# Performance work log

Measured on AMD Instinct MI355X. Metric: run time of the kernel, lower is better.

## Reference

```python
import jax, jax.numpy as jnp
import numpy as np

H = 128   # hidden_size
B = 8
TQ = 512  # num queries
TK = 512  # num keys


def setup_inputs() -> dict:
    key = jax.random.key(0)
    ks = jax.random.split(key, 8)
    s = 1.0 / np.sqrt(H)  # torch Linear default init bound
    return {
        "queries": jax.random.normal(ks[0], (B, TQ, H), dtype=jnp.float32),
        "keys": jax.random.normal(ks[1], (B, TK, H), dtype=jnp.float32),
        "Wa_w": jax.random.uniform(ks[2], (H, H), jnp.float32, -s, s),
        "Wa_b": jax.random.uniform(ks[3], (H,), jnp.float32, -s, s),
        "Ua_w": jax.random.uniform(ks[4], (H, H), jnp.float32, -s, s),
        "Ua_b": jax.random.uniform(ks[5], (H,), jnp.float32, -s, s),
        "Va_w": jax.random.uniform(ks[6], (H,), jnp.float32, -s, s),
        "Va_b": jax.random.uniform(ks[7], (), jnp.float32, -s, s),
    }


def reference(queries, keys, Wa_w, Wa_b, Ua_w, Ua_b, Va_w, Va_b):
    # Linear projections (torch Linear: y = x @ W.T + b)
    q = queries @ Wa_w.T + Wa_b                  # (B, Tq, H)
    k = keys @ Ua_w.T + Ua_b                     # (B, Tk, H)
    # Additive (Bahdanau) scores with broadcast intermediate (B, Tq, Tk, H)
    e = jnp.tanh(q[:, :, None, :] + k[:, None, :, :])
    scores = jnp.einsum('bqkh,h->bqk', e, Va_w) + Va_b  # (B, Tq, Tk)
    weights = jax.nn.softmax(scores, axis=-1)            # softmax over keys
    contexts = jnp.einsum('bqk,bkh->bqh', weights, keys) # (B, Tq, H)
    return contexts, weights
```

## Files before the change

kernel.cpp:

```cpp
#include <hip/hip_runtime.h>
#include <hip/hip_bf16.h>
#include <stdint.h>

#define HD 128
#define NB 8
#define TQN 512
#define TKN 512
#define QT 8
#define KTILE 64
#define KSTR 132
#define QSTR 132
#define KBSTR 136

typedef __attribute__((ext_vector_type(8))) short short8;
typedef __attribute__((ext_vector_type(4))) float f32x4;
typedef __attribute__((ext_vector_type(2))) float f32x2;

#if __has_builtin(__builtin_elementwise_fma)
#define FMA2(a,b,c) __builtin_elementwise_fma((a),(b),(c))
#else
#define FMA2(a,b,c) ((a)*(b)+(c))
#endif

static __device__ __forceinline__ float lo16(uint32_t w){
  union { uint32_t i; float f; } v; v.i = w << 16; return v.f;
}
static __device__ __forceinline__ float hi16(uint32_t w){
  union { uint32_t i; float f; } v; v.i = w & 0xffff0000u; return v.f;
}
static __device__ __forceinline__ float bf2f(unsigned short u){
  union { uint32_t i; float f; } v; v.i = ((uint32_t)u) << 16; return v.f;
}
static __device__ __forceinline__ uint32_t f2bf(float f){
  union { float f; uint32_t i; } v; v.f = f;
  uint32_t u = v.i;
  u += 0x7fffu + ((u >> 16) & 1u);
  return u >> 16;
}
static __device__ __forceinline__ float tanh_acc(float x){
  float e = __builtin_amdgcn_exp2f(x * 2.8853900817779268f);
  return fmaf(-2.0f, __builtin_amdgcn_rcpf(e + 1.0f), 1.0f);
}
template<int CTRL>
static __device__ __forceinline__ float dpp_add(float x){
  union { float f; int i; } u; u.f = x;
  int y = __builtin_amdgcn_update_dpp(0, u.i, CTRL, 0xf, 0xf, true);
  union { int i; float f; } w; w.i = y;
  return x + w.f;
}
static __device__ __forceinline__ float ld1(const void* p, size_t idx, bool f32){
  return f32 ? ((const float*)p)[idx] : bf2f(((const unsigned short*)p)[idx]);
}
static __device__ __forceinline__ short8 ld8bf(const void* p, size_t idx, bool f32){
  short8 r;
  if (f32){
    const float* s = (const float*)p + idx;
    #pragma unroll
    for (int i = 0; i < 8; i++) r[i] = (short)f2bf(s[i]);
  } else {
    r = *(const short8*)((const unsigned short*)p + idx);
  }
  return r;
}

__global__ __launch_bounds__(256) void proj_kernel(
    const void* __restrict__ queries, const void* __restrict__ keys,
    const void* __restrict__ Wa_w,   const void* __restrict__ Wa_b,
    const void* __restrict__ Ua_w,   const void* __restrict__ Ua_b,
    float* __restrict__ tq_g, float* __restrict__ tk_g)
{
  __shared__ unsigned int flg_s[8];
  const int tid = threadIdx.x;
  if (tid < 8) flg_s[tid] = 0;
  __syncthreads();
  {
    const void* ptrs[6] = {queries, keys, Wa_w, Wa_b, Ua_w, Ua_b};
    const int grp = tid >> 5;
    const int l   = tid & 31;
    if (grp < 6){
      const unsigned short* p = (const unsigned short*)ptrs[grp];
      unsigned short a = p[2*l], c = p[64 + 2*l];
      if (((a >> 7) & 0xFF) > 0x90 || ((c >> 7) & 0xFF) > 0x90)
        atomicOr(&flg_s[grp], 1u);
    }
  }
  __syncthreads();
  const int lane = tid & 63, wv = tid >> 6, ln = lane & 15, quad = lane >> 4;
  const int b7  = blockIdx.x & 7;
  const int idx = blockIdx.x >> 3;
  const int row0 = (idx < 32) ? (b7*TQN + idx*16)
                              : (NB*TQN + b7*TKN + (idx-32)*16);

  const void* x; const void* W; const void* bias; float* dst; int r;
  bool fx, fw, fb;
  if (row0 < NB*TQN){
    x = queries; W = Wa_w; bias = Wa_b; dst = tq_g; r = row0;
    fx = flg_s[0] != 0; fw = flg_s[2] != 0; fb = flg_s[3] != 0;
  } else {
    x = keys; W = Ua_w; bias = Ua_b; dst = tk_g; r = row0 - NB*TQN;
    fx = flg_s[1] != 0; fw = flg_s[4] != 0; fb = flg_s[5] != 0;
  }

  short8 a[4];
  #pragma unroll
  for (int ks = 0; ks < 4; ks++)
    a[ks] = ld8bf(x, (size_t)(r + ln)*HD + ks*32 + quad*8, fx);

  #pragma unroll
  for (int nt = 0; nt < 2; nt++){
    const int h0 = (2*wv + nt)*16;
    f32x4 c = {0.f,0.f,0.f,0.f};
    #pragma unroll
    for (int ks = 0; ks < 4; ks++)
      c = __builtin_amdgcn_mfma_f32_16x16x32_bf16(
            a[ks], ld8bf(W, (size_t)(h0 + ln)*HD + ks*32 + quad*8, fw), c, 0,0,0);
    const float wb = ld1(bias, h0 + ln, fb);
    #pragma unroll
    for (int r4 = 0; r4 < 4; r4++){
      const float e = __builtin_amdgcn_exp2f((c[r4] + wb) * 2.8853900817779268f);
      dst[(size_t)(r + quad*4 + r4)*HD + h0 + ln] =
          fminf(fmaxf(e, 0x1p-13f), 0x1p13f);
    }
  }
}

__global__ __launch_bounds__(512, 4) void attn_kernel(
    const void* __restrict__ queries, const void* __restrict__ keys,
    const void* __restrict__ Va_w,
    const float* __restrict__ tq_g, const float* __restrict__ tk_g,
    void* __restrict__ out)
{
  __shared__ __align__(16) float tk_s[KTILE*KSTR];
  __shared__ float sc_s[QT*TKN];
  __shared__ unsigned int flg_s[4];

  const int tid = threadIdx.x;
  const int b     = blockIdx.x & 7;
  const int qbase = (blockIdx.x >> 3) * QT;

  float4 st[4];
  {
    const float4* src = (const float4*)(tk_g + (size_t)(b*TKN)*HD);
    #pragma unroll
    for (int j = 0; j < 4; j++) st[j] = src[tid + 512*j];
  }

  if (tid < 4) flg_s[tid] = 0;
  __syncthreads();
  {
    const void* ptrs[3] = {queries, keys, Va_w};
    const int grp = tid >> 5;
    const int l   = tid & 31;
    if (grp < 3){
      const unsigned short* p = (const unsigned short*)ptrs[grp];
      unsigned short a = p[2*l], c = p[64 + 2*l];
      if (((a >> 7) & 0xFF) > 0x90 || ((c >> 7) & 0xFF) > 0x90)
        atomicOr(&flg_s[grp], 1u);
    }
  }
  __syncthreads();
  const bool fQ  = flg_s[0] != 0;
  const bool fK  = flg_s[1] != 0;
  const bool fVw = flg_s[2] != 0;

  const int lane = tid & 63;
  const int wv   = tid >> 6;
  const int ln   = lane & 15;
  const int quad = lane >> 4;
  const int s8   = lane >> 3;
  const int o8   = lane & 7;

  f32x2 eq2[8], a2[8];
  {
    const float* qsrc = tq_g + (size_t)(b*TQN + qbase + wv)*HD + o8*16;
    #pragma unroll
    for (int c = 0; c < 4; c++){
      const float4 t = *(const float4*)(qsrc + c*4);
      eq2[2*c].x = t.x; eq2[2*c].y = t.y;
      eq2[2*c+1].x = t.z; eq2[2*c+1].y = t.w;
      a2[2*c].x   = -2.0f * ld1(Va_w, o8*16 + c*4 + 0, fVw);
      a2[2*c].y   = -2.0f * ld1(Va_w, o8*16 + c*4 + 1, fVw);
      a2[2*c+1].x = -2.0f * ld1(Va_w, o8*16 + c*4 + 2, fVw);
      a2[2*c+1].y = -2.0f * ld1(Va_w, o8*16 + c*4 + 3, fVw);
    }
  }
  f32x2 one2; one2.x = 1.f; one2.y = 1.f;

  float sc8[8];
  for (int kt = 0; kt < 8; kt++){
    #pragma unroll
    for (int j = 0; j < 4; j++){
      const int f = tid + 512*j;
      *(float4*)(tk_s + (f >> 5)*KSTR + (f & 31)*4) = st[j];
    }
    __syncthreads();
    if (kt < 7){
      const float4* src = (const float4*)(tk_g + (size_t)(b*TKN + (kt+1)*KTILE)*HD);
      #pragma unroll
      for (int j = 0; j < 4; j++) st[j] = src[tid + 512*j];
    }

    float acc[8];
    #pragma unroll
    for (int i = 0; i < 8; i++){
      const float* tk = tk_s + (i*8 + s8)*KSTR + o8*16;
      float acci = 0.f;
      #pragma unroll
      for (int c = 0; c < 4; c++){
        const float4 kv = *(const float4*)(tk + c*4);
        f32x2 kv0; kv0.x = kv.x; kv0.y = kv.y;
        f32x2 kv1; kv1.x = kv.z; kv1.y = kv.w;
        f32x2 x01 = FMA2(eq2[2*c],   kv0, one2);
        f32x2 x23 = FMA2(eq2[2*c+1], kv1, one2);
        f32x2 xs01; xs01.x = x01.y; xs01.y = x01.x;
        f32x2 xs23; xs23.x = x23.y; xs23.y = x23.x;
        f32x2 s01 = a2[2*c]   * xs01;
        f32x2 s23 = a2[2*c+1] * xs23;
        const float p01 = x01.x * x01.y;
        const float p23 = x23.x * x23.y;
        const float n01 = s01.x + s01.y;
        const float n23 = s23.x + s23.y;
        const float P   = p01 * p23;
        const float N   = fmaf(n01, p23, n23 * p01);
        acci = fmaf(N, __builtin_amdgcn_rcpf(P), acci);
      }
      acc[i] = acci;
    }
    #pragma unroll
    for (int i = 0; i < 8; i++){
      float a = acc[i];
      a = dpp_add<0xB1>(a);
      a = dpp_add<0x4E>(a);
      a = dpp_add<0x141>(a);
      acc[i] = a;
    }
    float sc = acc[0];
    #pragma unroll
    for (int i = 1; i < 8; i++) sc = (o8 == i) ? acc[i] : sc;
    sc8[kt] = sc;
    __syncthreads();
  }

  {
    float m = sc8[0];
    #pragma unroll
    for (int j = 1; j < 8; j++) m = fmaxf(m, sc8[j]);
    #pragma unroll
    for (int o = 32; o > 0; o >>= 1) m = fmaxf(m, __shfl_xor(m, o));
    float sum = 0.f;
    #pragma unroll
    for (int j = 0; j < 8; j++){
      sc8[j] = __builtin_amdgcn_exp2f((sc8[j]-m)*1.4426950408889634f);
      sum += sc8[j];
    }
    #pragma unroll
    for (int o = 32; o > 0; o >>= 1) sum += __shfl_xor(sum, o);
    const float inv = __builtin_amdgcn_rcpf(sum);
    const int psrc = ((((lane & 7) << 3) | (lane >> 3)) << 2);
    const size_t wbase = (size_t)NB*TQN*HD + (size_t)(b*TQN + qbase + wv)*TKN;
    #pragma unroll
    for (int j = 0; j < 8; j++){
      union { float f; int i; } u; u.f = sc8[j]*inv;
      union { int i; float f; } t; t.i = __builtin_amdgcn_ds_bpermute(psrc, u.i);
      sc_s[wv*TKN + j*64 + lane] = t.f;
      if (fQ) ((float*)out)[wbase + j*64 + lane] = t.f;
      else    ((unsigned short*)out)[wbase + j*64 + lane] = (unsigned short)f2bf(t.f);
    }
  }
  __syncthreads();

  {
    const int p2 = wv & 3;
    const int g2 = wv >> 2;
    const int h0 = ln * 8;
    f32x2 a0v[4], a1v[4];
    #pragma unroll
    for (int t = 0; t < 4; t++){
      a0v[t].x = 0.f; a0v[t].y = 0.f;
      a1v[t].x = 0.f; a1v[t].y = 0.f;
    }
    const float* w0rb = sc_s + (2*p2)*TKN + g2*32;
    if (!fK){
      const unsigned short* kb = (const unsigned short*)keys
          + (size_t)(b*TKN + g2*32)*HD + h0;
      for (int kt = 0; kt < 8; kt++){
        const float* w0r = w0rb + kt*KTILE;
        const float* w1r = w0r + TKN;
        #pragma unroll
        for (int i = 0; i < 8; i++){
          const int k = i*4 + quad;
          const uint4 v = *(const uint4*)(kb + (size_t)(kt*KTILE + k)*HD);
          const float w0 = w0r[k];
          const float w1 = w1r[k];
          f32x2 c0; c0.x = lo16(v.x); c0.y = hi16(v.x);
          f32x2 c1; c1.x = lo16(v.y); c1.y = hi16(v.y);
          f32x2 c2; c2.x = lo16(v.z); c2.y = hi16(v.z);
          f32x2 c3; c3.x = lo16(v.w); c3.y = hi16(v.w);
          f32x2 w0v; w0v.x = w0; w0v.y = w0;
          f32x2 w1v; w1v.x = w1; w1v.y = w1;
          a0v[0] = FMA2(w0v, c0, a0v[0]); a0v[1] = FMA2(w0v, c1, a0v[1]);
          a0v[2] = FMA2(w0v, c2, a0v[2]); a0v[3] = FMA2(w0v, c3, a0v[3]);
          a1v[0] = FMA2(w1v, c0, a1v[0]); a1v[1] = FMA2(w1v, c1, a1v[1]);
          a1v[2] = FMA2(w1v, c2, a1v[2]); a1v[3] = FMA2(w1v, c3, a1v[3]);
        }
      }
    } else {
      const float* kb = (const float*)keys + (size_t)(b*TKN + g2*32)*HD + h0;
      for (int kt = 0; kt < 8; kt++){
        const float* w0r = w0rb + kt*KTILE;
        const float* w1r = w0r + TKN;
        #pragma unroll
        for (int i = 0; i < 8; i++){
          const int k = i*4 + quad;
          const float* kr = kb + (size_t)(kt*KTILE + k)*HD;
          const float4 k0 = *(const float4*)(kr);
          const float4 k1 = *(const float4*)(kr + 4);
          const float w0 = w0r[k];
          const float w1 = w1r[k];
          f32x2 c0; c0.x = k0.x; c0.y = k0.y;
          f32x2 c1; c1.x = k0.z; c1.y = k0.w;
          f32x2 c2; c2.x = k1.x; c2.y = k1.y;
          f32x2 c3; c3.x = k1.z; c3.y = k1.w;
          f32x2 w0v; w0v.x = w0; w0v.y = w0;
          f32x2 w1v; w1v.x = w1; w1v.y = w1;
          a0v[0] = FMA2(w0v, c0, a0v[0]); a0v[1] = FMA2(w0v, c1, a0v[1]);
          a0v[2] = FMA2(w0v, c2, a0v[2]); a0v[3] = FMA2(w0v, c3, a0v[3]);
          a1v[0] = FMA2(w1v, c0, a1v[0]); a1v[1] = FMA2(w1v, c1, a1v[1]);
          a1v[2] = FMA2(w1v, c2, a1v[2]); a1v[3] = FMA2(w1v, c3, a1v[3]);
        }
      }
    }
    float a0[8], a1[8];
    #pragma unroll
    for (int t = 0; t < 4; t++){
      a0[2*t] = a0v[t].x; a0[2*t+1] = a0v[t].y;
      a1[2*t] = a1v[t].x; a1[2*t+1] = a1v[t].y;
    }
    #pragma unroll
    for (int t = 0; t < 8; t++){
      a0[t] += __shfl_xor(a0[t], 16); a0[t] += __shfl_xor(a0[t], 32);
      a1[t] += __shfl_xor(a1[t], 16); a1[t] += __shfl_xor(a1[t], 32);
    }
    __syncthreads();
    float* part = sc_s;
    if (g2 == 1 && quad == 0){
      *(float4*)(part + (2*p2  )*HD + h0    ) = (float4){a0[0],a0[1],a0[2],a0[3]};
      *(float4*)(part + (2*p2  )*HD + h0 + 4) = (float4){a0[4],a0[5],a0[6],a0[7]};
      *(float4*)(part + (2*p2+1)*HD + h0    ) = (float4){a1[0],a1[1],a1[2],a1[3]};
      *(float4*)(part + (2*p2+1)*HD + h0 + 4) = (float4){a1[4],a1[5],a1[6],a1[7]};
    }
    __syncthreads();
    if (g2 == 0 && quad == 0){
      const float4 p00 = *(const float4*)(part + (2*p2  )*HD + h0    );
      const float4 p01 = *(const float4*)(part + (2*p2  )*HD + h0 + 4);
      const float4 p10 = *(const float4*)(part + (2*p2+1)*HD + h0    );
      const float4 p11 = *(const float4*)(part + (2*p2+1)*HD + h0 + 4);
      const size_t crow0 = (size_t)(b*TQN + qbase + 2*p2    )*HD + h0;
      const size_t crow1 = (size_t)(b*TQN + qbase + 2*p2 + 1)*HD + h0;
      if (fQ){
        float* oc = (float*)out;
        *(float4*)(oc + crow0)     = (float4){a0[0]+p00.x, a0[1]+p00.y, a0[2]+p00.z, a0[3]+p00.w};
        *(float4*)(oc + crow0 + 4) = (float4){a0[4]+p01.x, a0[5]+p01.y, a0[6]+p01.z, a0[7]+p01.w};
        *(float4*)(oc + crow1)     = (float4){a1[0]+p10.x, a1[1]+p10.y, a1[2]+p10.z, a1[3]+p10.w};
        *(float4*)(oc + crow1 + 4) = (float4){a1[4]+p11.x, a1[5]+p11.y, a1[6]+p11.z, a1[7]+p11.w};
      } else {
        uint4 o0, o1;
        o0.x = f2bf(a0[0]+p00.x) | (f2bf(a0[1]+p00.y) << 16);
        o0.y = f2bf(a0[2]+p00.z) | (f2bf(a0[3]+p00.w) << 16);
        o0.z = f2bf(a0[4]+p01.x) | (f2bf(a0[5]+p01.y) << 16);
        o0.w = f2bf(a0[6]+p01.z) | (f2bf(a0[7]+p01.w) << 16);
        o1.x = f2bf(a1[0]+p10.x) | (f2bf(a1[1]+p10.y) << 16);
        o1.y = f2bf(a1[2]+p10.z) | (f2bf(a1[3]+p10.w) << 16);
        o1.z = f2bf(a1[4]+p11.x) | (f2bf(a1[5]+p11.y) << 16);
        o1.w = f2bf(a1[6]+p11.z) | (f2bf(a1[7]+p11.w) << 16);
        *(uint4*)((unsigned short*)out + crow0) = o0;
        *(uint4*)((unsigned short*)out + crow1) = o1;
      }
    }
  }
}

__global__ __launch_bounds__(512, 4) void fused_kernel(
    const void* __restrict__ queries, const void* __restrict__ keys,
    const void* __restrict__ Wa_w,   const void* __restrict__ Wa_b,
    const void* __restrict__ Ua_w,   const void* __restrict__ Ua_b,
    const void* __restrict__ Va_w,
    void* __restrict__ out)
{
  __shared__ float qp_s[QT*QSTR];
  __shared__ float va_s[HD];
  __shared__ __align__(16) unsigned short keys_s[KTILE*KBSTR];
  __shared__ __align__(16) float kp_s[KTILE*KSTR];
  __shared__ float sc_s[QT*TKN];
  __shared__ unsigned int flg_s[8];

  const int tid = threadIdx.x;
  if (tid < 8) flg_s[tid] = 0;
  __syncthreads();
  {
    const void* ptrs[7] = {queries, keys, Wa_w, Wa_b, Ua_w, Ua_b, Va_w};
    const int grp = tid >> 5;
    const int l   = tid & 31;
    if (grp < 7){
      const unsigned short* p = (const unsigned short*)ptrs[grp];
      unsigned short a = p[2*l], c = p[64 + 2*l];
      if (((a >> 7) & 0xFF) > 0x90 || ((c >> 7) & 0xFF) > 0x90)
        atomicOr(&flg_s[grp], 1u);
    }
  }
  __syncthreads();
  const bool fQ  = flg_s[0] != 0;
  const bool fK  = flg_s[1] != 0;
  const bool fWw = flg_s[2] != 0;
  const bool fWb = flg_s[3] != 0;
  const bool fUw = flg_s[4] != 0;
  const bool fUb = flg_s[5] != 0;
  const bool fVw = flg_s[6] != 0;

  const int lane = tid & 63;
  const int wv   = tid >> 6;
  const int ln   = lane & 15;
  const int quad = lane >> 4;
  const int b     = blockIdx.x >> 6;
  const int qbase = (blockIdx.x & 63) * QT;

  if (tid < HD) va_s[tid] = ld1(Va_w, tid, fVw);
  {
    const int h0 = wv * 16;
    const size_t qrow = (size_t)(b*TQN + qbase + (ln & 7))*HD;
    f32x4 c = {0.f,0.f,0.f,0.f};
    #pragma unroll
    for (int ks = 0; ks < 4; ks++){
      short8 a = ld8bf(queries, qrow + ks*32 + quad*8, fQ);
      short8 w = ld8bf(Wa_w, (size_t)(h0 + ln)*HD + ks*32 + quad*8, fWw);
      c = __builtin_amdgcn_mfma_f32_16x16x32_bf16(a, w, c, 0,0,0);
    }
    const float wb = ld1(Wa_b, h0 + ln, fWb);
    #pragma unroll
    for (int r = 0; r < 4; r++){
      const int row = quad*4 + r;
      if (row < QT) qp_s[row*QSTR + h0 + ln] = tanh_acc(c[r] + wb);
    }
  }
  short8 ub[4];
  float ubias;
  {
    const int h0 = wv * 16;
    #pragma unroll
    for (int ks = 0; ks < 4; ks++)
      ub[ks] = ld8bf(Ua_w, (size_t)(h0 + ln)*HD + ks*32 + quad*8, fUw);
    ubias = ld1(Ua_b, h0 + ln, fUb);
  }
  {
    if (fK){
      const float4* src = (const float4*)((const float*)keys + (size_t)(b*TKN)*HD);
      #pragma unroll
      for (int j = 0; j < 4; j++){
        const int f = tid + 512*j;
        float4 v = src[f];
        const int k = f >> 5, h = (f & 31)*4;
        uint2 p;
        p.x = f2bf(v.x) | (f2bf(v.y) << 16);
        p.y = f2bf(v.z) | (f2bf(v.w) << 16);
        *(uint2*)(keys_s + k*KBSTR + h) = p;
      }
    } else {
      const uint4* src = (const uint4*)((const unsigned short*)keys + (size_t)(b*TKN)*HD);
      #pragma unroll
      for (int j = 0; j < 2; j++){
        const int f = tid + 512*j;
        uint4 v = src[f];
        const int k = f >> 4, h = (f & 15)*8;
        *(uint4*)(keys_s + k*KBSTR + h) = v;
      }
    }
  }
  __syncthreads();

  const int s8 = lane >> 3;
  const int o8 = lane & 7;
  float tqr[16], var[16], vat[16];
  {
    const float* qsrc = qp_s + wv*QSTR + o8*16;
    const float* vsrc = va_s + o8*16;
    #pragma unroll
    for (int c = 0; c < 4; c++){
      float4 t = *(const float4*)(qsrc + c*4);
      float4 v = *(const float4*)(vsrc + c*4);
      tqr[c*4+0]=t.x; tqr[c*4+1]=t.y; tqr[c*4+2]=t.z; tqr[c*4+3]=t.w;
      var[c*4+0]=v.x; var[c*4+1]=v.y; var[c*4+2]=v.z; var[c*4+3]=v.w;
      vat[c*4+0]=v.x*t.x; vat[c*4+1]=v.y*t.y; vat[c*4+2]=v.z*t.z; vat[c*4+3]=v.w*t.w;
    }
  }
  for (int kt = 0; kt < 8; kt++){
    f32x4 kc[4];
    #pragma unroll
    for (int mt = 0; mt < 4; mt++) kc[mt] = (f32x4){0.f,0.f,0.f,0.f};
    #pragma unroll
    for (int ks = 0; ks < 4; ks++){
      short8 af[4];
      #pragma unroll
      for (int mt = 0; mt < 4; mt++)
        af[mt] = *(const short8*)(keys_s + (mt*16 + ln)*KBSTR + ks*32 + quad*8);
      #pragma unroll
      for (int mt = 0; mt < 4; mt++)
        kc[mt] = __builtin_amdgcn_mfma_f32_16x16x32_bf16(af[mt], ub[ks], kc[mt], 0,0,0);
    }
    __syncthreads();
    #pragma unroll
    for (int mt = 0; mt < 4; mt++)
      #pragma unroll
      for (int r = 0; r < 4; r++)
        kp_s[(mt*16 + quad*4 + r)*KSTR + wv*16 + ln] = tanh_acc(kc[mt][r] + ubias);
    if (kt < 7){
      if (fK){
        const float4* src = (const float4*)((const float*)keys + (size_t)(b*TKN + (kt+1)*KTILE)*HD);
        #pragma unroll
        for (int j = 0; j < 4; j++){
          const int f = tid + 512*j;
          float4 v = src[f];
          const int k = f >> 5, h = (f & 31)*4;
          uint2 p;
          p.x = f2bf(v.x) | (f2bf(v.y) << 16);
          p.y = f2bf(v.z) | (f2bf(v.w) << 16);
          *(uint2*)(keys_s + k*KBSTR + h) = p;
        }
      } else {
        const uint4* src = (const uint4*)((const unsigned short*)keys + (size_t)(b*TKN + (kt+1)*KTILE)*HD);
        #pragma unroll
        for (int j = 0; j < 2; j++){
          const int f = tid + 512*j;
          uint4 v = src[f];
          const int k = f >> 4, h = (f & 15)*8;
          *(uint4*)(keys_s + k*KBSTR + h) = v;
        }
      }
    }
    __syncthreads();
    float acc[8];
    #pragma unroll
    for (int i = 0; i < 8; i++) acc[i] = 0.f;
    #pragma unroll
    for (int i = 0; i < 8; i++){
      const float* tk = kp_s + (i*8 + s8)*KSTR + o8*16;
      #pragma unroll
      for (int c = 0; c < 4; c++){
        const float4 kv = *(const float4*)(tk + c*4);
        acc[i] = fmaf(fmaf(var[c*4+0], kv.x, vat[c*4+0]),
                      __builtin_amdgcn_rcpf(fmaf(tqr[c*4+0], kv.x, 1.f)), acc[i]);
        acc[i] = fmaf(fmaf(var[c*4+1], kv.y, vat[c*4+1]),
                      __builtin_amdgcn_rcpf(fmaf(tqr[c*4+1], kv.y, 1.f)), acc[i]);
        acc[i] = fmaf(fmaf(var[c*4+2], kv.z, vat[c*4+2]),
                      __builtin_amdgcn_rcpf(fmaf(tqr[c*4+2], kv.z, 1.f)), acc[i]);
        acc[i] = fmaf(fmaf(var[c*4+3], kv.w, vat[c*4+3]),
                      __builtin_amdgcn_rcpf(fmaf(tqr[c*4+3], kv.w, 1.f)), acc[i]);
      }
    }
    #pragma unroll
    for (int i = 0; i < 8; i++){
      float a = acc[i];
      a = dpp_add<0xB1>(a);
      a = dpp_add<0x4E>(a);
      a = dpp_add<0x141>(a);
      acc[i] = a;
    }
    float sc = acc[0];
    #pragma unroll
    for (int i = 1; i < 8; i++) sc = (o8 == i) ? acc[i] : sc;
    sc_s[wv*TKN + kt*KTILE + o8*8 + s8] = sc;
  }
  __syncthreads();
  {
    float vals[8];
    float m = -1e30f;
    #pragma unroll
    for (int j = 0; j < 8; j++){
      vals[j] = sc_s[wv*TKN + lane + 64*j];
      m = fmaxf(m, vals[j]);
    }
    #pragma unroll
    for (int o = 32; o > 0; o >>= 1) m = fmaxf(m, __shfl_xor(m, o));
    float sum = 0.f;
    #pragma unroll
    for (int j = 0; j < 8; j++){
      vals[j] = __builtin_amdgcn_exp2f((vals[j]-m)*1.4426950408889634f);
      sum += vals[j];
    }
    #pragma unroll
    for (int o = 32; o > 0; o >>= 1) sum += __shfl_xor(sum, o);
    const float inv = __builtin_amdgcn_rcpf(sum);
    const size_t wbase = (size_t)NB*TQN*HD + (size_t)(b*TQN + qbase + wv)*TKN;
    #pragma unroll
    for (int j = 0; j < 8; j++){
      const float w = vals[j]*inv;
      sc_s[wv*TKN + lane + 64*j] = w;
      if (fQ) ((float*)out)[wbase + lane + 64*j] = w;
      else    ((unsigned short*)out)[wbase + lane + 64*j] = (unsigned short)f2bf(w);
    }
  }
  __syncthreads();
  {
    const int p2 = wv & 3;
    const int g2 = wv >> 2;
    const int h0 = ln * 8;
    float a0[8], a1[8];
    #pragma unroll
    for (int t = 0; t < 8; t++){ a0[t] = 0.f; a1[t] = 0.f; }
    for (int kt = 0; kt < 8; kt++){
      if (fK){
        const float4* src = (const float4*)((const float*)keys + (size_t)(b*TKN + kt*KTILE)*HD);
        #pragma unroll
        for (int j = 0; j < 4; j++){
          const int f = tid + 512*j;
          const int k = f >> 5, h = (f & 31)*4;
          *(float4*)(kp_s + k*KSTR + h) = src[f];
        }
      } else {
        const uint4* src = (const uint4*)((const unsigned short*)keys + (size_t)(b*TKN + kt*KTILE)*HD);
        #pragma unroll
        for (int j = 0; j < 2; j++){
          const int f = tid + 512*j;
          const int k = f >> 4, h = (f & 15)*8;
          uint4 v = src[f];
          float4 d0, d1;
          d0.x = lo16(v.x); d0.y = hi16(v.x); d0.z = lo16(v.y); d0.w = hi16(v.y);
          d1.x = lo16(v.z); d1.y = hi16(v.z); d1.z = lo16(v.w); d1.w = hi16(v.w);
          *(float4*)(kp_s + k*KSTR + h)     = d0;
          *(float4*)(kp_s + k*KSTR + h + 4) = d1;
        }
      }
      __syncthreads();
      const float* w0r = sc_s + (2*p2)*TKN + kt*KTILE + g2*32;
      const float* w1r = w0r + TKN;
      #pragma unroll
      for (int i = 0; i < 8; i++){
        const int k = i*4 + quad;
        const float w0 = w0r[k];
        const float w1 = w1r[k];
        const float* kr = kp_s + (g2*32 + k)*KSTR + h0;
        const float4 k0 = *(const float4*)(kr);
        const float4 k1 = *(const float4*)(kr + 4);
        a0[0]=fmaf(w0,k0.x,a0[0]); a0[1]=fmaf(w0,k0.y,a0[1]);
        a0[2]=fmaf(w0,k0.z,a0[2]); a0[3]=fmaf(w0,k0.w,a0[3]);
        a0[4]=fmaf(w0,k1.x,a0[4]); a0[5]=fmaf(w0,k1.y,a0[5]);
        a0[6]=fmaf(w0,k1.z,a0[6]); a0[7]=fmaf(w0,k1.w,a0[7]);
        a1[0]=fmaf(w1,k0.x,a1[0]); a1[1]=fmaf(w1,k0.y,a1[1]);
        a1[2]=fmaf(w1,k0.z,a1[2]); a1[3]=fmaf(w1,k0.w,a1[3]);
        a1[4]=fmaf(w1,k1.x,a1[4]); a1[5]=fmaf(w1,k1.y,a1[5]);
        a1[6]=fmaf(w1,k1.z,a1[6]); a1[7]=fmaf(w1,k1.w,a1[7]);
      }
      __syncthreads();
    }
    #pragma unroll
    for (int t = 0; t < 8; t++){
      a0[t] += __shfl_xor(a0[t], 16); a0[t] += __shfl_xor(a0[t], 32);
      a1[t] += __shfl_xor(a1[t], 16); a1[t] += __shfl_xor(a1[t], 32);
    }
    float* part = qp_s;
    if (g2 == 1 && quad == 0){
      *(float4*)(part + (2*p2  )*HD + h0    ) = (float4){a0[0],a0[1],a0[2],a0[3]};
      *(float4*)(part + (2*p2  )*HD + h0 + 4) = (float4){a0[4],a0[5],a0[6],a0[7]};
      *(float4*)(part + (2*p2+1)*HD + h0    ) = (float4){a1[0],a1[1],a1[2],a1[3]};
      *(float4*)(part + (2*p2+1)*HD + h0 + 4) = (float4){a1[4],a1[5],a1[6],a1[7]};
    }
    __syncthreads();
    if (g2 == 0 && quad == 0){
      const float4 p00 = *(const float4*)(part + (2*p2  )*HD + h0    );
      const float4 p01 = *(const float4*)(part + (2*p2  )*HD + h0 + 4);
      const float4 p10 = *(const float4*)(part + (2*p2+1)*HD + h0    );
      const float4 p11 = *(const float4*)(part + (2*p2+1)*HD + h0 + 4);
      const size_t crow0 = (size_t)(b*TQN + qbase + 2*p2    )*HD + h0;
      const size_t crow1 = (size_t)(b*TQN + qbase + 2*p2 + 1)*HD + h0;
      if (fQ){
        float* oc = (float*)out;
        *(float4*)(oc + crow0)     = (float4){a0[0]+p00.x, a0[1]+p00.y, a0[2]+p00.z, a0[3]+p00.w};
        *(float4*)(oc + crow0 + 4) = (float4){a0[4]+p01.x, a0[5]+p01.y, a0[6]+p01.z, a0[7]+p01.w};
        *(float4*)(oc + crow1)     = (float4){a1[0]+p10.x, a1[1]+p10.y, a1[2]+p10.z, a1[3]+p10.w};
        *(float4*)(oc + crow1 + 4) = (float4){a1[4]+p11.x, a1[5]+p11.y, a1[6]+p11.z, a1[7]+p11.w};
      } else {
        uint4 o0, o1;
        o0.x = f2bf(a0[0]+p00.x) | (f2bf(a0[1]+p00.y) << 16);
        o0.y = f2bf(a0[2]+p00.z) | (f2bf(a0[3]+p00.w) << 16);
        o0.z = f2bf(a0[4]+p01.x) | (f2bf(a0[5]+p01.y) << 16);
        o0.w = f2bf(a0[6]+p01.z) | (f2bf(a0[7]+p01.w) << 16);
        o1.x = f2bf(a1[0]+p10.x) | (f2bf(a1[1]+p10.y) << 16);
        o1.y = f2bf(a1[2]+p10.z) | (f2bf(a1[3]+p10.w) << 16);
        o1.z = f2bf(a1[4]+p11.x) | (f2bf(a1[5]+p11.y) << 16);
        o1.w = f2bf(a1[6]+p11.z) | (f2bf(a1[7]+p11.w) << 16);
        *(uint4*)((unsigned short*)out + crow0) = o0;
        *(uint4*)((unsigned short*)out + crow1) = o1;
      }
    }
  }
}

extern "C" void kernel_launch(void* const* d_in, const int* in_sizes, int n_in,
                              void* d_out, int out_size, void* d_ws, size_t ws_size,
                              hipStream_t stream) {
  (void)in_sizes; (void)n_in; (void)out_size;
  const size_t need = (size_t)2 * NB * TQN * HD * sizeof(float);
  if (ws_size >= need){
    float* tq_g = (float*)d_ws;
    float* tk_g = tq_g + (size_t)NB*TQN*HD;
    proj_kernel<<<512, 256, 0, stream>>>(d_in[0], d_in[1], d_in[2], d_in[3],
                                         d_in[4], d_in[5], tq_g, tk_g);
    attn_kernel<<<512, 512, 0, stream>>>(d_in[0], d_in[1], d_in[6],
                                         tq_g, tk_g, d_out);
  } else {
    fused_kernel<<<512, 512, 0, stream>>>(d_in[0], d_in[1], d_in[2], d_in[3],
                                          d_in[4], d_in[5], d_in[6], d_out);
  }
}
```

Baseline: 151.2 us.

## Halve queries per block, split hidden dim across waves, drop score LDS buffer

```diff
diff --git a/kernel.cpp b/kernel.cpp
--- a/kernel.cpp
+++ b/kernel.cpp
@@ -6,11 +6,13 @@
 #define NB 8
 #define TQN 512
 #define TKN 512
-#define QT 8
+#define QT 4
 #define KTILE 64
 #define KSTR 132
 #define QSTR 132
 #define KBSTR 136
+#define FQT 8
+#define WGT_OFF 2048
 
 typedef __attribute__((ext_vector_type(8))) short short8;
 typedef __attribute__((ext_vector_type(4))) float f32x4;
@@ -124,14 +126,13 @@
   }
 }
 
-__global__ __launch_bounds__(512, 4) void attn_kernel(
+__global__ __launch_bounds__(512, 8) void attn_kernel(
     const void* __restrict__ queries, const void* __restrict__ keys,
     const void* __restrict__ Va_w,
     const float* __restrict__ tq_g, const float* __restrict__ tk_g,
     void* __restrict__ out)
 {
   __shared__ __align__(16) float tk_s[KTILE*KSTR];
-  __shared__ float sc_s[QT*TKN];
   __shared__ unsigned int flg_s[4];
 
   const int tid = threadIdx.x;
@@ -165,23 +166,25 @@
 
   const int lane = tid & 63;
   const int wv   = tid >> 6;
+  const int qr   = wv & 3;
+  const int hh   = wv >> 2;
   const int ln   = lane & 15;
   const int quad = lane >> 4;
   const int s8   = lane >> 3;
   const int o8   = lane & 7;
 
-  f32x2 eq2[8], a2[8];
-  {
-    const float* qsrc = tq_g + (size_t)(b*TQN + qbase + wv)*HD + o8*16;
-    #pragma unroll
-    for (int c = 0; c < 4; c++){
+  f32x2 eq2[4], a2[4];
+  {
+    const float* qsrc = tq_g + (size_t)(b*TQN + qbase + qr)*HD + o8*16 + hh*8;
+    #pragma unroll
+    for (int c = 0; c < 2; c++){
       const float4 t = *(const float4*)(qsrc + c*4);
       eq2[2*c].x = t.x; eq2[2*c].y = t.y;
       eq2[2*c+1].x = t.z; eq2[2*c+1].y = t.w;
-      a2[2*c].x   = -2.0f * ld1(Va_w, o8*16 + c*4 + 0, fVw);
-      a2[2*c].y   = -2.0f * ld1(Va_w, o8*16 + c*4 + 1, fVw);
-      a2[2*c+1].x = -2.0f * ld1(Va_w, o8*16 + c*4 + 2, fVw);
-      a2[2*c+1].y = -2.0f * ld1(Va_w, o8*16 + c*4 + 3, fVw);
+      a2[2*c].x   = -2.0f * ld1(Va_w, o8*16 + hh*8 + c*4 + 0, fVw);
+      a2[2*c].y   = -2.0f * ld1(Va_w, o8*16 + hh*8 + c*4 + 1, fVw);
+      a2[2*c+1].x = -2.0f * ld1(Va_w, o8*16 + hh*8 + c*4 + 2, fVw);
+      a2[2*c+1].y = -2.0f * ld1(Va_w, o8*16 + hh*8 + c*4 + 3, fVw);
     }
   }
   f32x2 one2; one2.x = 1.f; one2.y = 1.f;
@@ -203,10 +206,10 @@
     float acc[8];
     #pragma unroll
     for (int i = 0; i < 8; i++){
-      const float* tk = tk_s + (i*8 + s8)*KSTR + o8*16;
+      const float* tk = tk_s + (i*8 + s8)*KSTR + o8*16 + hh*8;
       float acci = 0.f;
       #pragma unroll
-      for (int c = 0; c < 4; c++){
+      for (int c = 0; c < 2; c++){
         const float4 kv = *(const float4*)(tk + c*4);
         f32x2 kv0; kv0.x = kv.x; kv0.y = kv.y;
         f32x2 kv1; kv1.x = kv.z; kv1.y = kv.w;
@@ -241,28 +244,39 @@
     __syncthreads();
   }
 
-  {
-    float m = sc8[0];
-    #pragma unroll
-    for (int j = 1; j < 8; j++) m = fmaxf(m, sc8[j]);
+  if (hh == 1){
+    #pragma unroll
+    for (int kt = 0; kt < 8; kt++)
+      tk_s[qr*TKN + kt*64 + o8*8 + s8] = sc8[kt];
+  }
+  __syncthreads();
+  if (hh == 0){
+    float vals[8];
+    float m = -1e30f;
+    #pragma unroll
+    for (int j = 0; j < 8; j++){
+      vals[j] = sc8[j] + tk_s[qr*TKN + j*64 + o8*8 + s8];
+      m = fmaxf(m, vals[j]);
+    }
     #pragma unroll
     for (int o = 32; o > 0; o >>= 1) m = fmaxf(m, __shfl_xor(m, o));
     float sum = 0.f;
     #pragma unroll
     for (int j = 0; j < 8; j++){
-      sc8[j] = __builtin_amdgcn_exp2f((sc8[j]-m)*1.4426950408889634f);
-      sum += sc8[j];
+      vals[j] = __builtin_amdgcn_exp2f((vals[j]-m)*1.4426950408889634f);
+      sum += vals[j];
     }
     #pragma unroll
     for (int o = 32; o > 0; o >>= 1) sum += __shfl_xor(sum, o);
     const float inv = __builtin_amdgcn_rcpf(sum);
     const int psrc = ((((lane & 7) << 3) | (lane >> 3)) << 2);
-    const size_t wbase = (size_t)NB*TQN*HD + (size_t)(b*TQN + qbase + wv)*TKN;
+    const size_t wbase = (size_t)NB*TQN*HD + (size_t)(b*TQN + qbase + qr)*TKN;
+    float* wrow = tk_s + WGT_OFF + qr*TKN;
     #pragma unroll
     for (int j = 0; j < 8; j++){
-      union { float f; int i; } u; u.f = sc8[j]*inv;
+      union { float f; int i; } u; u.f = vals[j]*inv;
       union { int i; float f; } t; t.i = __builtin_amdgcn_ds_bpermute(psrc, u.i);
-      sc_s[wv*TKN + j*64 + lane] = t.f;
+      wrow[j*64 + lane] = t.f;
       if (fQ) ((float*)out)[wbase + j*64 + lane] = t.f;
       else    ((unsigned short*)out)[wbase + j*64 + lane] = (unsigned short)f2bf(t.f);
     }
@@ -270,8 +284,8 @@
   __syncthreads();
 
   {
-    const int p2 = wv & 3;
-    const int g2 = wv >> 2;
+    const int p2 = wv & 1;
+    const int g2 = wv >> 1;
     const int h0 = ln * 8;
     f32x2 a0v[4], a1v[4];
     #pragma unroll
@@ -279,15 +293,17 @@
       a0v[t].x = 0.f; a0v[t].y = 0.f;
       a1v[t].x = 0.f; a1v[t].y = 0.f;
     }
-    const float* w0rb = sc_s + (2*p2)*TKN + g2*32;
+    const float* w0rb = tk_s + WGT_OFF + (2*p2)*TKN;
     if (!fK){
       const unsigned short* kb = (const unsigned short*)keys
-          + (size_t)(b*TKN + g2*32)*HD + h0;
-      for (int kt = 0; kt < 8; kt++){
+          + (size_t)(b*TKN)*HD + h0;
+      #pragma unroll
+      for (int t = 0; t < 2; t++){
+        const int kt = g2*2 + t;
         const float* w0r = w0rb + kt*KTILE;
         const float* w1r = w0r + TKN;
         #pragma unroll
-        for (int i = 0; i < 8; i++){
+        for (int i = 0; i < 16; i++){
           const int k = i*4 + quad;
           const uint4 v = *(const uint4*)(kb + (size_t)(kt*KTILE + k)*HD);
           const float w0 = w0r[k];
@@ -305,12 +321,14 @@
         }
       }
     } else {
-      const float* kb = (const float*)keys + (size_t)(b*TKN + g2*32)*HD + h0;
-      for (int kt = 0; kt < 8; kt++){
+      const float* kb = (const float*)keys + (size_t)(b*TKN)*HD + h0;
+      #pragma unroll
+      for (int t = 0; t < 2; t++){
+        const int kt = g2*2 + t;
         const float* w0r = w0rb + kt*KTILE;
         const float* w1r = w0r + TKN;
         #pragma unroll
-        for (int i = 0; i < 8; i++){
+        for (int i = 0; i < 16; i++){
           const int k = i*4 + quad;
           const float* kr = kb + (size_t)(kt*KTILE + k)*HD;
           const float4 k0 = *(const float4*)(kr);
@@ -341,8 +359,330 @@
       a0[t] += __shfl_xor(a0[t], 16); a0[t] += __shfl_xor(a0[t], 32);
       a1[t] += __shfl_xor(a1[t], 16); a1[t] += __shfl_xor(a1[t], 32);
     }
+    float* part = tk_s;
+    if (g2 > 0 && quad == 0){
+      const int base = ((g2-1)*4 + 2*p2)*HD + h0;
+      *(float4*)(part + base       ) = (float4){a0[0],a0[1],a0[2],a0[3]};
+      *(float4*)(part + base + 4   ) = (float4){a0[4],a0[5],a0[6],a0[7]};
+      *(float4*)(part + base + HD  ) = (float4){a1[0],a1[1],a1[2],a1[3]};
+      *(float4*)(part + base + HD+4) = (float4){a1[4],a1[5],a1[6],a1[7]};
+    }
     __syncthreads();
-    float* part = sc_s;
+    if (g2 == 0 && quad == 0){
+      #pragma unroll
+      for (int gg = 0; gg < 3; gg++){
+        const int base = (gg*4 + 2*p2)*HD + h0;
+        const float4 q00 = *(const float4*)(part + base);
+        const float4 q01 = *(const float4*)(part + base + 4);
+        const float4 q10 = *(const float4*)(part + base + HD);
+        const float4 q11 = *(const float4*)(part + base + HD + 4);
+        a0[0]+=q00.x; a0[1]+=q00.y; a0[2]+=q00.z; a0[3]+=q00.w;
+        a0[4]+=q01.x; a0[5]+=q01.y; a0[6]+=q01.z; a0[7]+=q01.w;
+        a1[0]+=q10.x; a1[1]+=q10.y; a1[2]+=q10.z; a1[3]+=q10.w;
+        a1[4]+=q11.x; a1[5]+=q11.y; a1[6]+=q11.z; a1[7]+=q11.w;
+      }
+      const size_t crow0 = (size_t)(b*TQN + qbase + 2*p2    )*HD + h0;
+      const size_t crow1 = (size_t)(b*TQN + qbase + 2*p2 + 1)*HD + h0;
+      if (fQ){
+        float* oc = (float*)out;
+        *(float4*)(oc + crow0)     = (float4){a0[0],a0[1],a0[2],a0[3]};
+        *(float4*)(oc + crow0 + 4) = (float4){a0[4],a0[5],a0[6],a0[7]};
+        *(float4*)(oc + crow1)     = (float4){a1[0],a1[1],a1[2],a1[3]};
+        *(float4*)(oc + crow1 + 4) = (float4){a1[4],a1[5],a1[6],a1[7]};
+      } else {
+        uint4 o0, o1;
+        o0.x = f2bf(a0[0]) | (f2bf(a0[1]) << 16);
+        o0.y = f2bf(a0[2]) | (f2bf(a0[3]) << 16);
+        o0.z = f2bf(a0[4]) | (f2bf(a0[5]) << 16);
+        o0.w = f2bf(a0[6]) | (f2bf(a0[7]) << 16);
+        o1.x = f2bf(a1[0]) | (f2bf(a1[1]) << 16);
+        o1.y = f2bf(a1[2]) | (f2bf(a1[3]) << 16);
+        o1.z = f2bf(a1[4]) | (f2bf(a1[5]) << 16);
+        o1.w = f2bf(a1[6]) | (f2bf(a1[7]) << 16);
+        *(uint4*)((unsigned short*)out + crow0) = o0;
+        *(uint4*)((unsigned short*)out + crow1) = o1;
+      }
+    }
+  }
+}
+
+__global__ __launch_bounds__(512, 4) void fused_kernel(
+    const void* __restrict__ queries, const void* __restrict__ keys,
+    const void* __restrict__ Wa_w,   const void* __restrict__ Wa_b,
+    const void* __restrict__ Ua_w,   const void* __restrict__ Ua_b,
+    const void* __restrict__ Va_w,
+    void* __restrict__ out)
+{
+  __shared__ float qp_s[FQT*QSTR];
+  __shared__ float va_s[HD];
+  __shared__ __align__(16) unsigned short keys_s[KTILE*KBSTR];
+  __shared__ __align__(16) float kp_s[KTILE*QSTR];
+  __shared__ float sc_s[FQT*TKN];
+  __shared__ unsigned int flg_s[8];
+
+  const int tid = threadIdx.x;
+  if (tid < 8) flg_s[tid] = 0;
+  __syncthreads();
+  {
+    const void* ptrs[7] = {queries, keys, Wa_w, Wa_b, Ua_w, Ua_b, Va_w};
+    const int grp = tid >> 5;
+    const int l   = tid & 31;
+    if (grp < 7){
+      const unsigned short* p = (const unsigned short*)ptrs[grp];
+      unsigned short a = p[2*l], c = p[64 + 2*l];
+      if (((a >> 7) & 0xFF) > 0x90 || ((c >> 7) & 0xFF) > 0x90)
+        atomicOr(&flg_s[grp], 1u);
+    }
+  }
+  __syncthreads();
+  const bool fQ  = flg_s[0] != 0;
+  const bool fK  = flg_s[1] != 0;
+  const bool fWw = flg_s[2] != 0;
+  const bool fWb = flg_s[3] != 0;
+  const bool fUw = flg_s[4] != 0;
+  const bool fUb = flg_s[5] != 0;
+  const bool fVw = flg_s[6] != 0;
+
+  const int lane = tid & 63;
+  const int wv   = tid >> 6;
+  const int ln   = lane & 15;
+  const int quad = lane >> 4;
+  const int b     = blockIdx.x >> 6;
+  const int qbase = (blockIdx.x & 63) * FQT;
+
+  if (tid < HD) va_s[tid] = ld1(Va_w, tid, fVw);
+  {
+    const int h0 = wv * 16;
+    const size_t qrow = (size_t)(b*TQN + qbase + (ln & 7))*HD;
+    f32x4 c = {0.f,0.f,0.f,0.f};
+    #pragma unroll
+    for (int ks = 0; ks < 4; ks++){
+      short8 a = ld8bf(queries, qrow + ks*32 + quad*8, fQ);
+      short8 w = ld8bf(Wa_w, (size_t)(h0 + ln)*HD + ks*32 + quad*8, fWw);
+      c = __builtin_amdgcn_mfma_f32_16x16x32_bf16(a, w, c, 0,0,0);
+    }
+    const float wb = ld1(Wa_b, h0 + ln, fWb);
+    #pragma unroll
+    for (int r = 0; r < 4; r++){
+      const int row = quad*4 + r;
+      if (row < FQT) qp_s[row*QSTR + h0 + ln] = tanh_acc(c[r] + wb);
+    }
+  }
+  short8 ub[4];
+  float ubias;
+  {
+    const int h0 = wv * 16;
+    #pragma unroll
+    for (int ks = 0; ks < 4; ks++)
+      ub[ks] = ld8bf(Ua_w, (size_t)(h0 + ln)*HD + ks*32 + quad*8, fUw);
+    ubias = ld1(Ua_b, h0 + ln, fUb);
+  }
+  {
+    if (fK){
+      const float4* src = (const float4*)((const float*)keys + (size_t)(b*TKN)*HD);
+      #pragma unroll
+      for (int j = 0; j < 4; j++){
+        const int f = tid + 512*j;
+        float4 v = src[f];
+        const int k = f >> 5, h = (f & 31)*4;
+        uint2 p;
+        p.x = f2bf(v.x) | (f2bf(v.y) << 16);
+        p.y = f2bf(v.z) | (f2bf(v.w) << 16);
+        *(uint2*)(keys_s + k*KBSTR + h) = p;
+      }
+    } else {
+      const uint4* src = (const uint4*)((const unsigned short*)keys + (size_t)(b*TKN)*HD);
+      #pragma unroll
+      for (int j = 0; j < 2; j++){
+        const int f = tid + 512*j;
+        uint4 v = src[f];
+        const int k = f >> 4, h = (f & 15)*8;
+        *(uint4*)(keys_s + k*KBSTR + h) = v;
+      }
+    }
+  }
+  __syncthreads();
+
+  const int s8 = lane >> 3;
+  const int o8 = lane & 7;
+  float tqr[16], var[16], vat[16];
+  {
+    const float* qsrc = qp_s + wv*QSTR + o8*16;
+    const float* vsrc = va_s + o8*16;
+    #pragma unroll
+    for (int c = 0; c < 4; c++){
+      float4 t = *(const float4*)(qsrc + c*4);
+      float4 v = *(const float4*)(vsrc + c*4);
+      tqr[c*4+0]=t.x; tqr[c*4+1]=t.y; tqr[c*4+2]=t.z; tqr[c*4+3]=t.w;
+      var[c*4+0]=v.x; var[c*4+1]=v.y; var[c*4+2]=v.z; var[c*4+3]=v.w;
+      vat[c*4+0]=v.x*t.x; vat[c*4+1]=v.y*t.y; vat[c*4+2]=v.z*t.z; vat[c*4+3]=v.w*t.w;
+    }
+  }
+  for (int kt = 0; kt < 8; kt++){
+    f32x4 kc[4];
+    #pragma unroll
+    for (int mt = 0; mt < 4; mt++) kc[mt] = (f32x4){0.f,0.f,0.f,0.f};
+    #pragma unroll
+    for (int ks = 0; ks < 4; ks++){
+      short8 af[4];
+      #pragma unroll
+      for (int mt = 0; mt < 4; mt++)
+        af[mt] = *(const short8*)(keys_s + (mt*16 + ln)*KBSTR + ks*32 + quad*8);
+      #pragma unroll
+      for (int mt = 0; mt < 4; mt++)
+        kc[mt] = __builtin_amdgcn_mfma_f32_16x16x32_bf16(af[mt], ub[ks], kc[mt], 0,0,0);
+    }
+    __syncthreads();
+    #pragma unroll
+    for (int mt = 0; mt < 4; mt++)
+      #pragma unroll
+      for (int r = 0; r < 4; r++)
+        kp_s[(mt*16 + quad*4 + r)*QSTR + wv*16 + ln] = tanh_acc(kc[mt][r] + ubias);
+    if (kt < 7){
+      if (fK){
+        const float4* src = (const float4*)((const float*)keys + (size_t)(b*TKN + (kt+1)*KTILE)*HD);
+        #pragma unroll
+        for (int j = 0; j < 4; j++){
+          const int f = tid + 512*j;
+          float4 v = src[f];
+          const int k = f >> 5, h = (f & 31)*4;
+          uint2 p;
+          p.x = f2bf(v.x) | (f2bf(v.y) << 16);
+          p.y = f2bf(v.z) | (f2bf(v.w) << 16);
+          *(uint2*)(keys_s + k*KBSTR + h) = p;
+        }
+      } else {
+        const uint4* src = (const uint4*)((const unsigned short*)keys + (size_t)(b*TKN + (kt+1)*KTILE)*HD);
+        #pragma unroll
+        for (int j = 0; j < 2; j++){
+          const int f = tid + 512*j;
+          uint4 v = src[f];
+          const int k = f >> 4, h = (f & 15)*8;
+          *(uint4*)(keys_s + k*KBSTR + h) = v;
+        }
+      }
+    }
+    __syncthreads();
+    float acc[8];
+    #pragma unroll
+    for (int i = 0; i < 8; i++) acc[i] = 0.f;
+    #pragma unroll
+    for (int i = 0; i < 8; i++){
+      const float* tk = kp_s + (i*8 + s8)*QSTR + o8*16;
+      #pragma unroll
+      for (int c = 0; c < 4; c++){
+        const float4 kv = *(const float4*)(tk + c*4);
+        acc[i] = fmaf(fmaf(var[c*4+0], kv.x, vat[c*4+0]),
+                      __builtin_amdgcn_rcpf(fmaf(tqr[c*4+0], kv.x, 1.f)), acc[i]);
+        acc[i] = fmaf(fmaf(var[c*4+1], kv.y, vat[c*4+1]),
+                      __builtin_amdgcn_rcpf(fmaf(tqr[c*4+1], kv.y, 1.f)), acc[i]);
+        acc[i] = fmaf(fmaf(var[c*4+2], kv.z, vat[c*4+2]),
+                      __builtin_amdgcn_rcpf(fmaf(tqr[c*4+2], kv.z, 1.f)), acc[i]);
+        acc[i] = fmaf(fmaf(var[c*4+3], kv.w, vat[c*4+3]),
+                      __builtin_amdgcn_rcpf(fmaf(tqr[c*4+3], kv.w, 1.f)), acc[i]);
+      }
+    }
+    #pragma unroll
+    for (int i = 0; i < 8; i++){
+      float a = acc[i];
+      a = dpp_add<0xB1>(a);
+      a = dpp_add<0x4E>(a);
+      a = dpp_add<0x141>(a);
+      acc[i] = a;
+    }
+    float sc = acc[0];
+    #pragma unroll
+    for (int i = 1; i < 8; i++) sc = (o8 == i) ? acc[i] : sc;
+    sc_s[wv*TKN + kt*KTILE + o8*8 + s8] = sc;
+  }
+  __syncthreads();
+  {
+    float vals[8];
+    float m = -1e30f;
+    #pragma unroll
+    for (int j = 0; j < 8; j++){
+      vals[j] = sc_s[wv*TKN + lane + 64*j];
+      m = fmaxf(m, vals[j]);
+    }
+    #pragma unroll
+    for (int o = 32; o > 0; o >>= 1) m = fmaxf(m, __shfl_xor(m, o));
+    float sum = 0.f;
+    #pragma unroll
+    for (int j = 0; j < 8; j++){
+      vals[j] = __builtin_amdgcn_exp2f((vals[j]-m)*1.4426950408889634f);
+      sum += vals[j];
+    }
+    #pragma unroll
+    for (int o = 32; o > 0; o >>= 1) sum += __shfl_xor(sum, o);
+    const float inv = __builtin_amdgcn_rcpf(sum);
+    const size_t wbase = (size_t)NB*TQN*HD + (size_t)(b*TQN + qbase + wv)*TKN;
+    #pragma unroll
+    for (int j = 0; j < 8; j++){
+      const float w = vals[j]*inv;
+      sc_s[wv*TKN + lane + 64*j] = w;
+      if (fQ) ((float*)out)[wbase + lane + 64*j] = w;
+      else    ((unsigned short*)out)[wbase + lane + 64*j] = (unsigned short)f2bf(w);
+    }
+  }
+  __syncthreads();
+  {
+    const int p2 = wv & 3;
+    const int g2 = wv >> 2;
+    const int h0 = ln * 8;
+    float a0[8], a1[8];
+    #pragma unroll
+    for (int t = 0; t < 8; t++){ a0[t] = 0.f; a1[t] = 0.f; }
+    for (int kt = 0; kt < 8; kt++){
+      if (fK){
+        const float4* src = (const float4*)((const float*)keys + (size_t)(b*TKN + kt*KTILE)*HD);
+        #pragma unroll
+        for (int j = 0; j < 4; j++){
+          const int f = tid + 512*j;
+          const int k = f >> 5, h = (f & 31)*4;
+          *(float4*)(kp_s + k*QSTR + h) = src[f];
+        }
+      } else {
+        const uint4* src = (const uint4*)((const unsigned short*)keys + (size_t)(b*TKN + kt*KTILE)*HD);
+        #pragma unroll
+        for (int j = 0; j < 2; j++){
+          const int f = tid + 512*j;
+          const int k = f >> 4, h = (f & 15)*8;
+          uint4 v = src[f];
+          float4 d0, d1;
+          d0.x = lo16(v.x); d0.y = hi16(v.x); d0.z = lo16(v.y); d0.w = hi16(v.y);
+          d1.x = lo16(v.z); d1.y = hi16(v.z); d1.z = lo16(v.w); d1.w = hi16(v.w);
+          *(float4*)(kp_s + k*QSTR + h)     = d0;
+          *(float4*)(kp_s + k*QSTR + h + 4) = d1;
+        }
+      }
+      __syncthreads();
+      const float* w0r = sc_s + (2*p2)*TKN + kt*KTILE + g2*32;
+      const float* w1r = w0r + TKN;
+      #pragma unroll
+      for (int i = 0; i < 8; i++){
+        const int k = i*4 + quad;
+        const float w0 = w0r[k];
+        const float w1 = w1r[k];
+        const float* kr = kp_s + (g2*32 + k)*QSTR + h0;
+        const float4 k0 = *(const float4*)(kr);
+        const float4 k1 = *(const float4*)(kr + 4);
+        a0[0]=fmaf(w0,k0.x,a0[0]); a0[1]=fmaf(w0,k0.y,a0[1]);
+        a0[2]=fmaf(w0,k0.z,a0[2]); a0[3]=fmaf(w0,k0.w,a0[3]);
+        a0[4]=fmaf(w0,k1.x,a0[4]); a0[5]=fmaf(w0,k1.y,a0[5]);
+        a0[6]=fmaf(w0,k1.z,a0[6]); a0[7]=fmaf(w0,k1.w,a0[7]);
+        a1[0]=fmaf(w1,k0.x,a1[0]); a1[1]=fmaf(w1,k0.y,a1[1]);
+        a1[2]=fmaf(w1,k0.z,a1[2]); a1[3]=fmaf(w1,k0.w,a1[3]);
+        a1[4]=fmaf(w1,k1.x,a1[4]); a1[5]=fmaf(w1,k1.y,a1[5]);
+        a1[6]=fmaf(w1,k1.z,a1[6]); a1[7]=fmaf(w1,k1.w,a1[7]);
+      }
+      __syncthreads();
+    }
+    #pragma unroll
+    for (int t = 0; t < 8; t++){
+      a0[t] += __shfl_xor(a0[t], 16); a0[t] += __shfl_xor(a0[t], 32);
+      a1[t] += __shfl_xor(a1[t], 16); a1[t] += __shfl_xor(a1[t], 32);
+    }
+    float* part = qp_s;
     if (g2 == 1 && quad == 0){
       *(float4*)(part + (2*p2  )*HD + h0    ) = (float4){a0[0],a0[1],a0[2],a0[3]};
       *(float4*)(part + (2*p2  )*HD + h0 + 4) = (float4){a0[4],a0[5],a0[6],a0[7]};
@@ -380,320 +720,6 @@
   }
 }
 
-__global__ __launch_bounds__(512, 4) void fused_kernel(
-    const void* __restrict__ queries, const void* __restrict__ keys,
-    const void* __restrict__ Wa_w,   const void* __restrict__ Wa_b,
-    const void* __restrict__ Ua_w,   const void* __restrict__ Ua_b,
-    const void* __restrict__ Va_w,
-    void* __restrict__ out)
-{
-  __shared__ float qp_s[QT*QSTR];
-  __shared__ float va_s[HD];
-  __shared__ __align__(16) unsigned short keys_s[KTILE*KBSTR];
-  __shared__ __align__(16) float kp_s[KTILE*KSTR];
-  __shared__ float sc_s[QT*TKN];
-  __shared__ unsigned int flg_s[8];
-
-  const int tid = threadIdx.x;
-  if (tid < 8) flg_s[tid] = 0;
-  __syncthreads();
-  {
-    const void* ptrs[7] = {queries, keys, Wa_w, Wa_b, Ua_w, Ua_b, Va_w};
-    const int grp = tid >> 5;
-    const int l   = tid & 31;
-    if (grp < 7){
-      const unsigned short* p = (const unsigned short*)ptrs[grp];
-      unsigned short a = p[2*l], c = p[64 + 2*l];
-      if (((a >> 7) & 0xFF) > 0x90 || ((c >> 7) & 0xFF) > 0x90)
-        atomicOr(&flg_s[grp], 1u);
-    }
-  }
-  __syncthreads();
-  const bool fQ  = flg_s[0] != 0;
-  const bool fK  = flg_s[1] != 0;
-  const bool fWw = flg_s[2] != 0;
-  const bool fWb = flg_s[3] != 0;
-  const bool fUw = flg_s[4] != 0;
-  const bool fUb = flg_s[5] != 0;
-  const bool fVw = flg_s[6] != 0;
-
-  const int lane = tid & 63;
-  const int wv   = tid >> 6;
-  const int ln   = lane & 15;
-  const int quad = lane >> 4;
-  const int b     = blockIdx.x >> 6;
-  const int qbase = (blockIdx.x & 63) * QT;
-
-  if (tid < HD) va_s[tid] = ld1(Va_w, tid, fVw);
-  {
-    const int h0 = wv * 16;
-    const size_t qrow = (size_t)(b*TQN + qbase + (ln & 7))*HD;
-    f32x4 c = {0.f,0.f,0.f,0.f};
-    #pragma unroll
-    for (int ks = 0; ks < 4; ks++){
-      short8 a = ld8bf(queries, qrow + ks*32 + quad*8, fQ);
-      short8 w = ld8bf(Wa_w, (size_t)(h0 + ln)*HD + ks*32 + quad*8, fWw);
-      c = __builtin_amdgcn_mfma_f32_16x16x32_bf16(a, w, c, 0,0,0);
-    }
-    const float wb = ld1(Wa_b, h0 + ln, fWb);
-    #pragma unroll
-    for (int r = 0; r < 4; r++){
-      const int row = quad*4 + r;
-      if (row < QT) qp_s[row*QSTR + h0 + ln] = tanh_acc(c[r] + wb);
-    }
-  }
-  short8 ub[4];
-  float ubias;
-  {
-    const int h0 = wv * 16;
-    #pragma unroll
-    for (int ks = 0; ks < 4; ks++)
-      ub[ks] = ld8bf(Ua_w, (size_t)(h0 + ln)*HD + ks*32 + quad*8, fUw);
-    ubias = ld1(Ua_b, h0 + ln, fUb);
-  }
-  {
-    if (fK){
-      const float4* src = (const float4*)((const float*)keys + (size_t)(b*TKN)*HD);
-      #pragma unroll
-      for (int j = 0; j < 4; j++){
-        const int f = tid + 512*j;
-        float4 v = src[f];
-        const int k = f >> 5, h = (f & 31)*4;
-        uint2 p;
-        p.x = f2bf(v.x) | (f2bf(v.y) << 16);
-        p.y = f2bf(v.z) | (f2bf(v.w) << 16);
-        *(uint2*)(keys_s + k*KBSTR + h) = p;
-      }
-    } else {
-      const uint4* src = (const uint4*)((const unsigned short*)keys + (size_t)(b*TKN)*HD);
-      #pragma unroll
-      for (int j = 0; j < 2; j++){
-        const int f = tid + 512*j;
-        uint4 v = src[f];
-        const int k = f >> 4, h = (f & 15)*8;
-        *(uint4*)(keys_s + k*KBSTR + h) = v;
-      }
-    }
-  }
-  __syncthreads();
-
-  const int s8 = lane >> 3;
-  const int o8 = lane & 7;
-  float tqr[16], var[16], vat[16];
-  {
-    const float* qsrc = qp_s + wv*QSTR + o8*16;
-    const float* vsrc = va_s + o8*16;
-    #pragma unroll
-    for (int c = 0; c < 4; c++){
-      float4 t = *(const float4*)(qsrc + c*4);
-      float4 v = *(const float4*)(vsrc + c*4);
-      tqr[c*4+0]=t.x; tqr[c*4+1]=t.y; tqr[c*4+2]=t.z; tqr[c*4+3]=t.w;
-      var[c*4+0]=v.x; var[c*4+1]=v.y; var[c*4+2]=v.z; var[c*4+3]=v.w;
-      vat[c*4+0]=v.x*t.x; vat[c*4+1]=v.y*t.y; vat[c*4+2]=v.z*t.z; vat[c*4+3]=v.w*t.w;
-    }
-  }
-  for (int kt = 0; kt < 8; kt++){
-    f32x4 kc[4];
-    #pragma unroll
-    for (int mt = 0; mt < 4; mt++) kc[mt] = (f32x4){0.f,0.f,0.f,0.f};
-    #pragma unroll
-    for (int ks = 0; ks < 4; ks++){
-      short8 af[4];
-      #pragma unroll
-      for (int mt = 0; mt < 4; mt++)
-        af[mt] = *(const short8*)(keys_s + (mt*16 + ln)*KBSTR + ks*32 + quad*8);
-      #pragma unroll
-      for (int mt = 0; mt < 4; mt++)
-        kc[mt] = __builtin_amdgcn_mfma_f32_16x16x32_bf16(af[mt], ub[ks], kc[mt], 0,0,0);
-    }
-    __syncthreads();
-    #pragma unroll
-    for (int mt = 0; mt < 4; mt++)
-      #pragma unroll
-      for (int r = 0; r < 4; r++)
-        kp_s[(mt*16 + quad*4 + r)*KSTR + wv*16 + ln] = tanh_acc(kc[mt][r] + ubias);
-    if (kt < 7){
-      if (fK){
-        const float4* src = (const float4*)((const float*)keys + (size_t)(b*TKN + (kt+1)*KTILE)*HD);
-        #pragma unroll
-        for (int j = 0; j < 4; j++){
-          const int f = tid + 512*j;
-          float4 v = src[f];
-          const int k = f >> 5, h = (f & 31)*4;
-          uint2 p;
-          p.x = f2bf(v.x) | (f2bf(v.y) << 16);
-          p.y = f2bf(v.z) | (f2bf(v.w) << 16);
-          *(uint2*)(keys_s + k*KBSTR + h) = p;
-        }
-      } else {
-        const uint4* src = (const uint4*)((const unsigned short*)keys + (size_t)(b*TKN + (kt+1)*KTILE)*HD);
-        #pragma unroll
-        for (int j = 0; j < 2; j++){
-          const int f = tid + 512*j;
-          uint4 v = src[f];
-          const int k = f >> 4, h = (f & 15)*8;
-          *(uint4*)(keys_s + k*KBSTR + h) = v;
-        }
-      }
-    }
-    __syncthreads();
-    float acc[8];
-    #pragma unroll
-    for (int i = 0; i < 8; i++) acc[i] = 0.f;
-    #pragma unroll
-    for (int i = 0; i < 8; i++){
-      const float* tk = kp_s + (i*8 + s8)*KSTR + o8*16;
-      #pragma unroll
-      for (int c = 0; c < 4; c++){
-        const float4 kv = *(const float4*)(tk + c*4);
-        acc[i] = fmaf(fmaf(var[c*4+0], kv.x, vat[c*4+0]),
-                      __builtin_amdgcn_rcpf(fmaf(tqr[c*4+0], kv.x, 1.f)), acc[i]);
-        acc[i] = fmaf(fmaf(var[c*4+1], kv.y, vat[c*4+1]),
-                      __builtin_amdgcn_rcpf(fmaf(tqr[c*4+1], kv.y, 1.f)), acc[i]);
-        acc[i] = fmaf(fmaf(var[c*4+2], kv.z, vat[c*4+2]),
-                      __builtin_amdgcn_rcpf(fmaf(tqr[c*4+2], kv.z, 1.f)), acc[i]);
-        acc[i] = fmaf(fmaf(var[c*4+3], kv.w, vat[c*4+3]),
-                      __builtin_amdgcn_rcpf(fmaf(tqr[c*4+3], kv.w, 1.f)), acc[i]);
-      }
-    }
-    #pragma unroll
-    for (int i = 0; i < 8; i++){
-      float a = acc[i];
-      a = dpp_add<0xB1>(a);
-      a = dpp_add<0x4E>(a);
-      a = dpp_add<0x141>(a);
-      acc[i] = a;
-    }
-    float sc = acc[0];
-    #pragma unroll
-    for (int i = 1; i < 8; i++) sc = (o8 == i) ? acc[i] : sc;
-    sc_s[wv*TKN + kt*KTILE + o8*8 + s8] = sc;
-  }
-  __syncthreads();
-  {
-    float vals[8];
-    float m = -1e30f;
-    #pragma unroll
-    for (int j = 0; j < 8; j++){
-      vals[j] = sc_s[wv*TKN + lane + 64*j];
-      m = fmaxf(m, vals[j]);
-    }
-    #pragma unroll
-    for (int o = 32; o > 0; o >>= 1) m = fmaxf(m, __shfl_xor(m, o));
-    float sum = 0.f;
-    #pragma unroll
-    for (int j = 0; j < 8; j++){
-      vals[j] = __builtin_amdgcn_exp2f((vals[j]-m)*1.4426950408889634f);
-      sum += vals[j];
-    }
-    #pragma unroll
-    for (int o = 32; o > 0; o >>= 1) sum += __shfl_xor(sum, o);
-    const float inv = __builtin_amdgcn_rcpf(sum);
-    const size_t wbase = (size_t)NB*TQN*HD + (size_t)(b*TQN + qbase + wv)*TKN;
-    #pragma unroll
-    for (int j = 0; j < 8; j++){
-      const float w = vals[j]*inv;
-      sc_s[wv*TKN + lane + 64*j] = w;
-      if (fQ) ((float*)out)[wbase + lane + 64*j] = w;
-      else    ((unsigned short*)out)[wbase + lane + 64*j] = (unsigned short)f2bf(w);
-    }
-  }
-  __syncthreads();
-  {
-    const int p2 = wv & 3;
-    const int g2 = wv >> 2;
-    const int h0 = ln * 8;
-    float a0[8], a1[8];
-    #pragma unroll
-    for (int t = 0; t < 8; t++){ a0[t] = 0.f; a1[t] = 0.f; }
-    for (int kt = 0; kt < 8; kt++){
-      if (fK){
-        const float4* src = (const float4*)((const float*)keys + (size_t)(b*TKN + kt*KTILE)*HD);
-        #pragma unroll
-        for (int j = 0; j < 4; j++){
-          const int f = tid + 512*j;
-          const int k = f >> 5, h = (f & 31)*4;
-          *(float4*)(kp_s + k*KSTR + h) = src[f];
-        }
-      } else {
-        const uint4* src = (const uint4*)((const unsigned short*)keys + (size_t)(b*TKN + kt*KTILE)*HD);
-        #pragma unroll
-        for (int j = 0; j < 2; j++){
-          const int f = tid + 512*j;
-          const int k = f >> 4, h = (f & 15)*8;
-          uint4 v = src[f];
-          float4 d0, d1;
-          d0.x = lo16(v.x); d0.y = hi16(v.x); d0.z = lo16(v.y); d0.w = hi16(v.y);
-          d1.x = lo16(v.z); d1.y = hi16(v.z); d1.z = lo16(v.w); d1.w = hi16(v.w);
-          *(float4*)(kp_s + k*KSTR + h)     = d0;
-          *(float4*)(kp_s + k*KSTR + h + 4) = d1;
-        }
-      }
-      __syncthreads();
-      const float* w0r = sc_s + (2*p2)*TKN + kt*KTILE + g2*32;
-      const float* w1r = w0r + TKN;
-      #pragma unroll
-      for (int i = 0; i < 8; i++){
-        const int k = i*4 + quad;
-        const float w0 = w0r[k];
-        const float w1 = w1r[k];
-        const float* kr = kp_s + (g2*32 + k)*KSTR + h0;
-        const float4 k0 = *(const float4*)(kr);
-        const float4 k1 = *(const float4*)(kr + 4);
-        a0[0]=fmaf(w0,k0.x,a0[0]); a0[1]=fmaf(w0,k0.y,a0[1]);
-        a0[2]=fmaf(w0,k0.z,a0[2]); a0[3]=fmaf(w0,k0.w,a0[3]);
-        a0[4]=fmaf(w0,k1.x,a0[4]); a0[5]=fmaf(w0,k1.y,a0[5]);
-        a0[6]=fmaf(w0,k1.z,a0[6]); a0[7]=fmaf(w0,k1.w,a0[7]);
-        a1[0]=fmaf(w1,k0.x,a1[0]); a1[1]=fmaf(w1,k0.y,a1[1]);
-        a1[2]=fmaf(w1,k0.z,a1[2]); a1[3]=fmaf(w1,k0.w,a1[3]);
-        a1[4]=fmaf(w1,k1.x,a1[4]); a1[5]=fmaf(w1,k1.y,a1[5]);
-        a1[6]=fmaf(w1,k1.z,a1[6]); a1[7]=fmaf(w1,k1.w,a1[7]);
-      }
-      __syncthreads();
-    }
-    #pragma unroll
-    for (int t = 0; t < 8; t++){
-      a0[t] += __shfl_xor(a0[t], 16); a0[t] += __shfl_xor(a0[t], 32);
-      a1[t] += __shfl_xor(a1[t], 16); a1[t] += __shfl_xor(a1[t], 32);
-    }
-    float* part = qp_s;
-    if (g2 == 1 && quad == 0){
-      *(float4*)(part + (2*p2  )*HD + h0    ) = (float4){a0[0],a0[1],a0[2],a0[3]};
-      *(float4*)(part + (2*p2  )*HD + h0 + 4) = (float4){a0[4],a0[5],a0[6],a0[7]};
-      *(float4*)(part + (2*p2+1)*HD + h0    ) = (float4){a1[0],a1[1],a1[2],a1[3]};
-      *(float4*)(part + (2*p2+1)*HD + h0 + 4) = (float4){a1[4],a1[5],a1[6],a1[7]};
-    }
-    __syncthreads();
-    if (g2 == 0 && quad == 0){
-      const float4 p00 = *(const float4*)(part + (2*p2  )*HD + h0    );
-      const float4 p01 = *(const float4*)(part + (2*p2  )*HD + h0 + 4);
-      const float4 p10 = *(const float4*)(part + (2*p2+1)*HD + h0    );
-      const float4 p11 = *(const float4*)(part + (2*p2+1)*HD + h0 + 4);
-      const size_t crow0 = (size_t)(b*TQN + qbase + 2*p2    )*HD + h0;
-      const size_t crow1 = (size_t)(b*TQN + qbase + 2*p2 + 1)*HD + h0;
-      if (fQ){
-        float* oc = (float*)out;
-        *(float4*)(oc + crow0)     = (float4){a0[0]+p00.x, a0[1]+p00.y, a0[2]+p00.z, a0[3]+p00.w};
-        *(float4*)(oc + crow0 + 4) = (float4){a0[4]+p01.x, a0[5]+p01.y, a0[6]+p01.z, a0[7]+p01.w};
-        *(float4*)(oc + crow1)     = (float4){a1[0]+p10.x, a1[1]+p10.y, a1[2]+p10.z, a1[3]+p10.w};
-        *(float4*)(oc + crow1 + 4) = (float4){a1[4]+p11.x, a1[5]+p11.y, a1[6]+p11.z, a1[7]+p11.w};
-      } else {
-        uint4 o0, o1;
-        o0.x = f2bf(a0[0]+p00.x) | (f2bf(a0[1]+p00.y) << 16);
-        o0.y = f2bf(a0[2]+p00.z) | (f2bf(a0[3]+p00.w) << 16);
-        o0.z = f2bf(a0[4]+p01.x) | (f2bf(a0[5]+p01.y) << 16);
-        o0.w = f2bf(a0[6]+p01.z) | (f2bf(a0[7]+p01.w) << 16);
-        o1.x = f2bf(a1[0]+p10.x) | (f2bf(a1[1]+p10.y) << 16);
-        o1.y = f2bf(a1[2]+p10.z) | (f2bf(a1[3]+p10.w) << 16);
-        o1.z = f2bf(a1[4]+p11.x) | (f2bf(a1[5]+p11.y) << 16);
-        o1.w = f2bf(a1[6]+p11.z) | (f2bf(a1[7]+p11.w) << 16);
-        *(uint4*)((unsigned short*)out + crow0) = o0;
-        *(uint4*)((unsigned short*)out + crow1) = o1;
-      }
-    }
-  }
-}
-
 extern "C" void kernel_launch(void* const* d_in, const int* in_sizes, int n_in,
                               void* d_out, int out_size, void* d_ws, size_t ws_size,
                               hipStream_t stream) {
@@ -704,8 +730,8 @@
     float* tk_g = tq_g + (size_t)NB*TQN*HD;
     proj_kernel<<<512, 256, 0, stream>>>(d_in[0], d_in[1], d_in[2], d_in[3],
                                          d_in[4], d_in[5], tq_g, tk_g);
-    attn_kernel<<<512, 512, 0, stream>>>(d_in[0], d_in[1], d_in[6],
-                                         tq_g, tk_g, d_out);
+    attn_kernel<<<1024, 512, 0, stream>>>(d_in[0], d_in[1], d_in[6],
+                                          tq_g, tk_g, d_out);
   } else {
     fused_kernel<<<512, 512, 0, stream>>>(d_in[0], d_in[1], d_in[2], d_in[3],
                                           d_in[4], d_in[5], d_in[6], d_out);
```

New measurement: 180.2 us. 19.2% more time.
